# Performance work log

Hardware: AMD Instinct MI355X
Metric: run time of the kernel (lower is better)

Reference implementation:

```python
import jax, jax.numpy as jnp
import numpy as np


def _lecun_tanh(x):
    return 1.7159 * jnp.tanh(0.666 * x)


def _lin_init(k, fan_in, fan_out):
    s = 1.0 / np.sqrt(fan_in)
    kw, kb = jax.random.split(k)
    W = jax.random.uniform(kw, (fan_in, fan_out), minval=-s, maxval=s, dtype=jnp.float32)
    b = jax.random.uniform(kb, (fan_out,), minval=-s, maxval=s, dtype=jnp.float32)
    return W, b


def setup_inputs() -> dict:
    key = jax.random.key(0)
    ks = jax.random.split(key, 8)
    B, T, OBS, H, A = 256, 1024, 32, 128, 8
    Wb, bb = _lin_init(ks[0], OBS + H, H)      # backbone Linear
    Wff1, bff1 = _lin_init(ks[1], H, H)
    Wff2, bff2 = _lin_init(ks[2], H, H)
    Wta, bta = _lin_init(ks[3], H, H)          # time_a
    Wtb, btb = _lin_init(ks[4], H, H)          # time_b
    Wa, ba = _lin_init(ks[5], H, A)            # actor head
    Wc, bc = _lin_init(ks[6], H, 1)            # critic head
    obs = jax.random.normal(ks[7], (B, T, OBS), dtype=jnp.float32)
    return dict(obs=obs, Wb=Wb, bb=bb, Wff1=Wff1, bff1=bff1, Wff2=Wff2, bff2=bff2,
                Wta=Wta, bta=bta, Wtb=Wtb, btb=btb, Wa=Wa, ba=ba, Wc=Wc, bc=bc)


def reference(obs, Wb, bb, Wff1, bff1, Wff2, bff2, Wta, bta, Wtb, btb, Wa, ba, Wc, bc):
    # CfCActorCritic.forward_sequence: CfC (default mode, 1 backbone layer, ts=1)
    # scanned over time, then actor/critic heads on every timestep output.
    B, T, _ = obs.shape
    H = Wff1.shape[0]
    ts = 1.0

    def step(h, x_t):
        z = jnp.concatenate([x_t, h], axis=-1)          # [B, OBS+H]
        z = _lecun_tanh(z @ Wb + bb)                    # backbone MLP
        ff1 = jnp.tanh(z @ Wff1 + bff1)
        ff2 = jnp.tanh(z @ Wff2 + bff2)
        t_interp = jax.nn.sigmoid((z @ Wta + bta) * ts + (z @ Wtb + btb))
        h_new = ff1 * (1.0 - t_interp) + t_interp * ff2
        return h_new, h_new

    h0 = jnp.zeros((B, H), dtype=obs.dtype)
    obs_t = jnp.swapaxes(obs, 0, 1)                     # [T, B, OBS]
    _, ys = jax.lax.scan(step, h0, obs_t)               # ys: [T, B, H]
    out = jnp.swapaxes(ys, 0, 1)                        # [B, T, H]
    mean = out @ Wa + ba                                # [B, T, A]
    value = (out @ Wc + bc).squeeze(-1)                 # [B, T]
    return mean, value
```

## Files before the change

kernel.cpp:

```cpp
#include <hip/hip_runtime.h>


typedef _Float16 half8 __attribute__((ext_vector_type(8)));
typedef float f32x4 __attribute__((ext_vector_type(4)));

#define T_STEPS 1024
#define OBS 32
#define H 128
#define A_DIM 8
#define NW 8
#define NT (NW * 64)
#define ROWS 4
#define NBLK 64

#define ZIN_P 168
#define ZF_P 136

__device__ __forceinline__ float fast_rcp(float x) { return __builtin_amdgcn_rcpf(x); }
__device__ __forceinline__ float fast_tanh(float x) {
    float e = __expf(2.0f * x);
    return 1.0f - 2.0f * fast_rcp(e + 1.0f);
}
__device__ __forceinline__ float fast_sigmoid(float x) {
    return fast_rcp(1.0f + __expf(-x));
}

__global__ void __launch_bounds__(NT) cfc_kernel(
    const float* __restrict__ obs,
    const float* __restrict__ Wb,  const float* __restrict__ bb,
    const float* __restrict__ Wff1, const float* __restrict__ bff1,
    const float* __restrict__ Wff2, const float* __restrict__ bff2,
    const float* __restrict__ Wta, const float* __restrict__ bta,
    const float* __restrict__ Wtb, const float* __restrict__ btb,
    const float* __restrict__ Wa,  const float* __restrict__ ba,
    const float* __restrict__ Wc,  const float* __restrict__ bc,
    float* __restrict__ out_mean, float* __restrict__ out_value)
{
    const int b0 = blockIdx.x * ROWS;
    const int tid = threadIdx.x;
    const int w = tid >> 6, l = tid & 63;
    const int lo = l & 15, hi = l >> 4;

    __shared__ _Float16 zin[16][ZIN_P];
    __shared__ _Float16 zf[16][ZF_P];

    const int colB = w * 16 + lo;

    half8 Bb[5];
#pragma unroll
    for (int ks = 0; ks < 5; ++ks)
#pragma unroll
        for (int j = 0; j < 8; ++j) {
            int k = ks * 32 + hi * 8 + j;
            Bb[ks][j] = (_Float16)Wb[k * H + colB];
        }
    const float bbv = bb[colB];

    half8 Bg0[4], Bg1[4], Bg2[4];
#pragma unroll
    for (int ks = 0; ks < 4; ++ks)
#pragma unroll
        for (int j = 0; j < 8; ++j) {
            int k = ks * 32 + hi * 8 + j;
            Bg0[ks][j] = (_Float16)Wff1[k * H + colB];
            Bg1[ks][j] = (_Float16)Wff2[k * H + colB];
            Bg2[ks][j] = (_Float16)(Wta[k * H + colB] + Wtb[k * H + colB]);
        }
    const float bg1 = bff1[colB], bg2 = bff2[colB], bg3 = bta[colB] + btb[colB];

    half8 Bh[4];
    float bh = 0.f;
    if (w == 7) {
#pragma unroll
        for (int ks = 0; ks < 4; ++ks)
#pragma unroll
            for (int j = 0; j < 8; ++j) {
                int k = ks * 32 + hi * 8 + j;
                float v = (lo < 8) ? Wa[k * A_DIM + lo] : ((lo == 8) ? Wc[k] : 0.0f);
                Bh[ks][j] = (_Float16)v;
            }
        bh = (lo < 8) ? ba[lo] : ((lo == 8) ? bc[0] : 0.0f);
    }

    for (int i = tid; i < 16 * ZIN_P; i += NT) (&zin[0][0])[i] = (_Float16)0.0f;
    __syncthreads();
    if (w == 0) {
        int r = l >> 5, c = l & 31;
        zin[r][c]     = (_Float16)obs[((size_t)(b0 + r) * T_STEPS) * OBS + c];
        zin[r + 2][c] = (_Float16)obs[((size_t)(b0 + r + 2) * T_STEPS) * OBS + c];
    }
    __syncthreads();

    float ox0 = 0.f, ox1 = 0.f;

    for (int t = 0; t < T_STEPS; ++t) {
        if (w == 0 && t + 1 < T_STEPS) {
            int r = l >> 5, c = l & 31;
            ox0 = obs[((size_t)(b0 + r) * T_STEPS + (t + 1)) * OBS + c];
            ox1 = obs[((size_t)(b0 + r + 2) * T_STEPS + (t + 1)) * OBS + c];
        }

        half8 A0 = *(const half8*)&zin[lo][0 * 32 + hi * 8];
        half8 A1 = *(const half8*)&zin[lo][1 * 32 + hi * 8];
        half8 A2 = *(const half8*)&zin[lo][2 * 32 + hi * 8];
        half8 A3 = *(const half8*)&zin[lo][3 * 32 + hi * 8];
        half8 A4 = *(const half8*)&zin[lo][4 * 32 + hi * 8];
        f32x4 accz = {0.f, 0.f, 0.f, 0.f};
        accz = __builtin_amdgcn_mfma_f32_16x16x32_f16(A0, Bb[0], accz, 0, 0, 0);
        accz = __builtin_amdgcn_mfma_f32_16x16x32_f16(A1, Bb[1], accz, 0, 0, 0);
        accz = __builtin_amdgcn_mfma_f32_16x16x32_f16(A2, Bb[2], accz, 0, 0, 0);
        accz = __builtin_amdgcn_mfma_f32_16x16x32_f16(A3, Bb[3], accz, 0, 0, 0);
        accz = __builtin_amdgcn_mfma_f32_16x16x32_f16(A4, Bb[4], accz, 0, 0, 0);

        if (w == 7 && t > 0) {
            f32x4 acch = {0.f, 0.f, 0.f, 0.f};
            acch = __builtin_amdgcn_mfma_f32_16x16x32_f16(A1, Bh[0], acch, 0, 0, 0);
            acch = __builtin_amdgcn_mfma_f32_16x16x32_f16(A2, Bh[1], acch, 0, 0, 0);
            acch = __builtin_amdgcn_mfma_f32_16x16x32_f16(A3, Bh[2], acch, 0, 0, 0);
            acch = __builtin_amdgcn_mfma_f32_16x16x32_f16(A4, Bh[3], acch, 0, 0, 0);
            if (hi == 0 && lo < 9) {
#pragma unroll
                for (int j = 0; j < 4; ++j) {
                    float v = acch[j] + bh;
                    if (lo < 8) out_mean[((size_t)(b0 + j) * T_STEPS + (t - 1)) * A_DIM + lo] = v;
                    else        out_value[(size_t)(b0 + j) * T_STEPS + (t - 1)] = v;
                }
            }
        }

#pragma unroll
        for (int j = 0; j < 4; ++j) {
            float zval = 1.7159f * fast_tanh(0.666f * (accz[j] + bbv));
            zf[hi * 4 + j][colB] = (_Float16)zval;
        }
        __syncthreads();

        half8 Z0 = *(const half8*)&zf[lo][0 * 32 + hi * 8];
        half8 Z1 = *(const half8*)&zf[lo][1 * 32 + hi * 8];
        half8 Z2 = *(const half8*)&zf[lo][2 * 32 + hi * 8];
        half8 Z3 = *(const half8*)&zf[lo][3 * 32 + hi * 8];
        f32x4 a1 = {0.f, 0.f, 0.f, 0.f}, a2 = a1, a3 = a1;
        a1 = __builtin_amdgcn_mfma_f32_16x16x32_f16(Z0, Bg0[0], a1, 0, 0, 0);
        a2 = __builtin_amdgcn_mfma_f32_16x16x32_f16(Z0, Bg1[0], a2, 0, 0, 0);
        a3 = __builtin_amdgcn_mfma_f32_16x16x32_f16(Z0, Bg2[0], a3, 0, 0, 0);
        a1 = __builtin_amdgcn_mfma_f32_16x16x32_f16(Z1, Bg0[1], a1, 0, 0, 0);
        a2 = __builtin_amdgcn_mfma_f32_16x16x32_f16(Z1, Bg1[1], a2, 0, 0, 0);
        a3 = __builtin_amdgcn_mfma_f32_16x16x32_f16(Z1, Bg2[1], a3, 0, 0, 0);
        a1 = __builtin_amdgcn_mfma_f32_16x16x32_f16(Z2, Bg0[2], a1, 0, 0, 0);
        a2 = __builtin_amdgcn_mfma_f32_16x16x32_f16(Z2, Bg1[2], a2, 0, 0, 0);
        a3 = __builtin_amdgcn_mfma_f32_16x16x32_f16(Z2, Bg2[2], a3, 0, 0, 0);
        a1 = __builtin_amdgcn_mfma_f32_16x16x32_f16(Z3, Bg0[3], a1, 0, 0, 0);
        a2 = __builtin_amdgcn_mfma_f32_16x16x32_f16(Z3, Bg1[3], a2, 0, 0, 0);
        a3 = __builtin_amdgcn_mfma_f32_16x16x32_f16(Z3, Bg2[3], a3, 0, 0, 0);

#pragma unroll
        for (int j = 0; j < 4; ++j) {
            float ff1 = fast_tanh(a1[j] + bg1);
            float ff2 = fast_tanh(a2[j] + bg2);
            float ti  = fast_sigmoid(a3[j] + bg3);
            float hv  = ff1 + ti * (ff2 - ff1);
            zin[hi * 4 + j][32 + colB] = (_Float16)hv;
        }

        if (w == 0 && t + 1 < T_STEPS) {
            int r = l >> 5, c = l & 31;
            zin[r][c]     = (_Float16)ox0;
            zin[r + 2][c] = (_Float16)ox1;
        }
        __syncthreads();
    }

    if (w == 7) {
        half8 A1 = *(const half8*)&zin[lo][32 + 0 * 32 + hi * 8];
        half8 A2 = *(const half8*)&zin[lo][32 + 1 * 32 + hi * 8];
        half8 A3 = *(const half8*)&zin[lo][32 + 2 * 32 + hi * 8];
        half8 A4 = *(const half8*)&zin[lo][32 + 3 * 32 + hi * 8];
        f32x4 acch = {0.f, 0.f, 0.f, 0.f};
        acch = __builtin_amdgcn_mfma_f32_16x16x32_f16(A1, Bh[0], acch, 0, 0, 0);
        acch = __builtin_amdgcn_mfma_f32_16x16x32_f16(A2, Bh[1], acch, 0, 0, 0);
        acch = __builtin_amdgcn_mfma_f32_16x16x32_f16(A3, Bh[2], acch, 0, 0, 0);
        acch = __builtin_amdgcn_mfma_f32_16x16x32_f16(A4, Bh[3], acch, 0, 0, 0);
        if (hi == 0 && lo < 9) {
#pragma unroll
            for (int j = 0; j < 4; ++j) {
                float v = acch[j] + bh;
                if (lo < 8) out_mean[((size_t)(b0 + j) * T_STEPS + (T_STEPS - 1)) * A_DIM + lo] = v;
                else        out_value[(size_t)(b0 + j) * T_STEPS + (T_STEPS - 1)] = v;
            }
        }
    }
}

extern "C" void kernel_launch(void* const* d_in, const int* in_sizes, int n_in,
                              void* d_out, int out_size, void* d_ws, size_t ws_size,
                              hipStream_t stream) {
    (void)in_sizes; (void)n_in; (void)d_ws; (void)ws_size; (void)out_size;
    const float* obs  = (const float*)d_in[0];
    const float* Wb   = (const float*)d_in[1];
    const float* bb   = (const float*)d_in[2];
    const float* Wff1 = (const float*)d_in[3];
    const float* bff1 = (const float*)d_in[4];
    const float* Wff2 = (const float*)d_in[5];
    const float* bff2 = (const float*)d_in[6];
    const float* Wta  = (const float*)d_in[7];
    const float* bta  = (const float*)d_in[8];
    const float* Wtb  = (const float*)d_in[9];
    const float* btb  = (const float*)d_in[10];
    const float* Wa   = (const float*)d_in[11];
    const float* ba   = (const float*)d_in[12];
    const float* Wc   = (const float*)d_in[13];
    const float* bc   = (const float*)d_in[14];
    float* out = (float*)d_out;
    float* out_mean  = out;
    float* out_value = out + (size_t)256 * 1024 * 8;

    cfc_kernel<<<dim3(NBLK), dim3(NT), 0, stream>>>(
        obs, Wb, bb, Wff1, bff1, Wff2, bff2, Wta, bta, Wtb, btb,
        Wa, ba, Wc, bc, out_mean, out_value);
}
```

Baseline: 1.159 ms.

## Shorten recurrent step critical path: split MFMA chain, fold biases, deeper obs prefetch

The backbone MFMA accumulation is split into two independent chains so consecutive MFMAs do not wait on each other. Biases are now folded into the initial accumulator values instead of being added after each matmul. The tanh and sigmoid activations are rewritten as exp2 with pre-scaled constants and fmaf, cutting per-element ALU work. The observation load is spread over two waves and prefetched two steps ahead, which hides global-load latency inside the serial time loop at the cost of a few extra registers.

```diff
diff --git a/kernel.cpp b/kernel.cpp
--- a/kernel.cpp
+++ b/kernel.cpp
@@ -16,14 +16,9 @@
 #define ZIN_P 168
 #define ZF_P 136
 
+#define L2E 1.44269504f
+
 __device__ __forceinline__ float fast_rcp(float x) { return __builtin_amdgcn_rcpf(x); }
-__device__ __forceinline__ float fast_tanh(float x) {
-    float e = __expf(2.0f * x);
-    return 1.0f - 2.0f * fast_rcp(e + 1.0f);
-}
-__device__ __forceinline__ float fast_sigmoid(float x) {
-    return fast_rcp(1.0f + __expf(-x));
-}
 
 __global__ void __launch_bounds__(NT) cfc_kernel(
     const float* __restrict__ obs,
@@ -84,36 +79,32 @@
 
     for (int i = tid; i < 16 * ZIN_P; i += NT) (&zin[0][0])[i] = (_Float16)0.0f;
     __syncthreads();
-    if (w == 0) {
-        int r = l >> 5, c = l & 31;
-        zin[r][c]     = (_Float16)obs[((size_t)(b0 + r) * T_STEPS) * OBS + c];
-        zin[r + 2][c] = (_Float16)obs[((size_t)(b0 + r + 2) * T_STEPS) * OBS + c];
-    }
+    const int rX = (w << 1) | (l >> 5), cX = l & 31;
+    if (w < 2) zin[rX][cX] = (_Float16)obs[((size_t)(b0 + rX) * T_STEPS) * OBS + cX];
     __syncthreads();
 
-    float ox0 = 0.f, ox1 = 0.f;
+    float oxA = 0.f, oxB = 0.f;
+    if (w < 2) {
+        oxA = obs[((size_t)(b0 + rX) * T_STEPS + 1) * OBS + cX];
+        oxB = obs[((size_t)(b0 + rX) * T_STEPS + 2) * OBS + cX];
+    }
 
     for (int t = 0; t < T_STEPS; ++t) {
-        if (w == 0 && t + 1 < T_STEPS) {
-            int r = l >> 5, c = l & 31;
-            ox0 = obs[((size_t)(b0 + r) * T_STEPS + (t + 1)) * OBS + c];
-            ox1 = obs[((size_t)(b0 + r + 2) * T_STEPS + (t + 1)) * OBS + c];
-        }
-
         half8 A0 = *(const half8*)&zin[lo][0 * 32 + hi * 8];
         half8 A1 = *(const half8*)&zin[lo][1 * 32 + hi * 8];
         half8 A2 = *(const half8*)&zin[lo][2 * 32 + hi * 8];
         half8 A3 = *(const half8*)&zin[lo][3 * 32 + hi * 8];
         half8 A4 = *(const half8*)&zin[lo][4 * 32 + hi * 8];
-        f32x4 accz = {0.f, 0.f, 0.f, 0.f};
-        accz = __builtin_amdgcn_mfma_f32_16x16x32_f16(A0, Bb[0], accz, 0, 0, 0);
-        accz = __builtin_amdgcn_mfma_f32_16x16x32_f16(A1, Bb[1], accz, 0, 0, 0);
-        accz = __builtin_amdgcn_mfma_f32_16x16x32_f16(A2, Bb[2], accz, 0, 0, 0);
-        accz = __builtin_amdgcn_mfma_f32_16x16x32_f16(A3, Bb[3], accz, 0, 0, 0);
-        accz = __builtin_amdgcn_mfma_f32_16x16x32_f16(A4, Bb[4], accz, 0, 0, 0);
+        f32x4 az0 = {bbv, bbv, bbv, bbv};
+        f32x4 az1 = {0.f, 0.f, 0.f, 0.f};
+        az0 = __builtin_amdgcn_mfma_f32_16x16x32_f16(A0, Bb[0], az0, 0, 0, 0);
+        az1 = __builtin_amdgcn_mfma_f32_16x16x32_f16(A1, Bb[1], az1, 0, 0, 0);
+        az0 = __builtin_amdgcn_mfma_f32_16x16x32_f16(A2, Bb[2], az0, 0, 0, 0);
+        az1 = __builtin_amdgcn_mfma_f32_16x16x32_f16(A3, Bb[3], az1, 0, 0, 0);
+        az0 = __builtin_amdgcn_mfma_f32_16x16x32_f16(A4, Bb[4], az0, 0, 0, 0);
 
         if (w == 7 && t > 0) {
-            f32x4 acch = {0.f, 0.f, 0.f, 0.f};
+            f32x4 acch = {bh, bh, bh, bh};
             acch = __builtin_amdgcn_mfma_f32_16x16x32_f16(A1, Bh[0], acch, 0, 0, 0);
             acch = __builtin_amdgcn_mfma_f32_16x16x32_f16(A2, Bh[1], acch, 0, 0, 0);
             acch = __builtin_amdgcn_mfma_f32_16x16x32_f16(A3, Bh[2], acch, 0, 0, 0);
@@ -121,17 +112,17 @@
             if (hi == 0 && lo < 9) {
 #pragma unroll
                 for (int j = 0; j < 4; ++j) {
-                    float v = acch[j] + bh;
-                    if (lo < 8) out_mean[((size_t)(b0 + j) * T_STEPS + (t - 1)) * A_DIM + lo] = v;
-                    else        out_value[(size_t)(b0 + j) * T_STEPS + (t - 1)] = v;
+                    if (lo < 8) out_mean[((size_t)(b0 + j) * T_STEPS + (t - 1)) * A_DIM + lo] = acch[j];
+                    else        out_value[(size_t)(b0 + j) * T_STEPS + (t - 1)] = acch[j];
                 }
             }
         }
 
 #pragma unroll
         for (int j = 0; j < 4; ++j) {
-            float zval = 1.7159f * fast_tanh(0.666f * (accz[j] + bbv));
-            zf[hi * 4 + j][colB] = (_Float16)zval;
+            float s = az0[j] + az1[j];
+            float r = fast_rcp(exp2f(1.9216697f * s) + 1.0f);
+            zf[hi * 4 + j][colB] = (_Float16)fmaf(-3.4318f, r, 1.7159f);
         }
         __syncthreads();
 
@@ -139,7 +130,9 @@
         half8 Z1 = *(const half8*)&zf[lo][1 * 32 + hi * 8];
         half8 Z2 = *(const half8*)&zf[lo][2 * 32 + hi * 8];
         half8 Z3 = *(const half8*)&zf[lo][3 * 32 + hi * 8];
-        f32x4 a1 = {0.f, 0.f, 0.f, 0.f}, a2 = a1, a3 = a1;
+        f32x4 a1 = {bg1, bg1, bg1, bg1};
+        f32x4 a2 = {bg2, bg2, bg2, bg2};
+        f32x4 a3 = {bg3, bg3, bg3, bg3};
         a1 = __builtin_amdgcn_mfma_f32_16x16x32_f16(Z0, Bg0[0], a1, 0, 0, 0);
         a2 = __builtin_amdgcn_mfma_f32_16x16x32_f16(Z0, Bg1[0], a2, 0, 0, 0);
         a3 = __builtin_amdgcn_mfma_f32_16x16x32_f16(Z0, Bg2[0], a3, 0, 0, 0);
@@ -155,17 +148,19 @@
 
 #pragma unroll
         for (int j = 0; j < 4; ++j) {
-            float ff1 = fast_tanh(a1[j] + bg1);
-            float ff2 = fast_tanh(a2[j] + bg2);
-            float ti  = fast_sigmoid(a3[j] + bg3);
-            float hv  = ff1 + ti * (ff2 - ff1);
-            zin[hi * 4 + j][32 + colB] = (_Float16)hv;
-        }
-
-        if (w == 0 && t + 1 < T_STEPS) {
-            int r = l >> 5, c = l & 31;
-            zin[r][c]     = (_Float16)ox0;
-            zin[r + 2][c] = (_Float16)ox1;
+            float r1 = fast_rcp(exp2f(2.8853901f * a1[j]) + 1.0f);
+            float ff1 = fmaf(-2.0f, r1, 1.0f);
+            float r2 = fast_rcp(exp2f(2.8853901f * a2[j]) + 1.0f);
+            float ff2 = fmaf(-2.0f, r2, 1.0f);
+            float ti = fast_rcp(1.0f + exp2f(-L2E * a3[j]));
+            zin[hi * 4 + j][32 + colB] = (_Float16)(ff1 + ti * (ff2 - ff1));
+        }
+
+        if (w < 2 && t + 1 < T_STEPS) {
+            zin[rX][cX] = (_Float16)oxA;
+            oxA = oxB;
+            const int tf = t + 3;
+            oxB = (tf < T_STEPS) ? obs[((size_t)(b0 + rX) * T_STEPS + tf) * OBS + cX] : 0.0f;
         }
         __syncthreads();
     }
@@ -175,7 +170,7 @@
         half8 A2 = *(const half8*)&zin[lo][32 + 1 * 32 + hi * 8];
         half8 A3 = *(const half8*)&zin[lo][32 + 2 * 32 + hi * 8];
         half8 A4 = *(const half8*)&zin[lo][32 + 3 * 32 + hi * 8];
-        f32x4 acch = {0.f, 0.f, 0.f, 0.f};
+        f32x4 acch = {bh, bh, bh, bh};
         acch = __builtin_amdgcn_mfma_f32_16x16x32_f16(A1, Bh[0], acch, 0, 0, 0);
         acch = __builtin_amdgcn_mfma_f32_16x16x32_f16(A2, Bh[1], acch, 0, 0, 0);
         acch = __builtin_amdgcn_mfma_f32_16x16x32_f16(A3, Bh[2], acch, 0, 0, 0);
@@ -183,9 +178,8 @@
         if (hi == 0 && lo < 9) {
 #pragma unroll
             for (int j = 0; j < 4; ++j) {
-                float v = acch[j] + bh;
-                if (lo < 8) out_mean[((size_t)(b0 + j) * T_STEPS + (T_STEPS - 1)) * A_DIM + lo] = v;
-                else        out_value[(size_t)(b0 + j) * T_STEPS + (T_STEPS - 1)] = v;
+                if (lo < 8) out_mean[((size_t)(b0 + j) * T_STEPS + (T_STEPS - 1)) * A_DIM + lo] = acch[j];
+                else        out_value[(size_t)(b0 + j) * T_STEPS + (T_STEPS - 1)] = acch[j];
             }
         }
     }
```

After: 1.303 ms. +12.4%, slower.
